# Optimization experiments

Measured on AMD Instinct MI355X. Metric: run time of the kernel, lower is better.

The kernel has to match this reference:

```python
import jax, jax.numpy as jnp
import numpy as np

B, N0, N1, FD, L, H = 4, 256, 256, 128, 3, 1
NG = N0 + N1            # nodes per graph
N = B * NG              # total nodes
EPS_BN = 1e-5
EPS_SM = 1e-16


def _build_edges():
    def perm_edges(n, off):
        idx = np.arange(n)
        a = np.repeat(idx, n); b = np.tile(idx, n)
        m = a != b
        return np.stack([a[m], b[m]]) + off
    e_intra = np.concatenate([perm_edges(N0, 0), perm_edges(N1, N0)], axis=1)
    a = np.arange(N0); b = np.arange(N0, N0 + N1)
    cross1 = np.stack([np.repeat(a, N1), np.tile(b, N0)])
    cross2 = np.stack([np.repeat(b, N0), np.tile(a, N1)])
    eg = np.concatenate([e_intra, cross1, cross2], axis=1)
    tg = np.concatenate([np.zeros(e_intra.shape[1], np.int32),
                         np.ones(cross1.shape[1] + cross2.shape[1], np.int32)])
    ei = np.concatenate([eg + g * NG for g in range(B)], axis=1).astype(np.int32)
    et = np.tile(tg, B).astype(np.int32)
    return jnp.asarray(ei), jnp.asarray(et)


def setup_inputs() -> dict:
    key = jax.random.key(0)
    ks = jax.random.split(key, 8)
    edge_index, edge_type = _build_edges()
    return {
        'desc0': jax.random.normal(ks[0], (B, FD, N0), jnp.float32),
        'desc1': jax.random.normal(ks[1], (B, FD, N1), jnp.float32),
        'W': jax.random.normal(ks[2], (L, 2, FD, H * FD), jnp.float32) * (1.0 / np.sqrt(FD)),
        'q': jax.random.normal(ks[3], (L, H * FD, H), jnp.float32) * 0.1,
        'k': jax.random.normal(ks[4], (L, H * FD, H), jnp.float32) * 0.1,
        'conv_b': jnp.zeros((L, FD), jnp.float32),
        'lin_W': jax.random.normal(ks[5], (L, FD, 2 * FD), jnp.float32) * (1.0 / np.sqrt(2 * FD)),
        'lin_b': jnp.zeros((L, FD), jnp.float32),
        'gamma': jnp.ones((L, FD), jnp.float32),
        'beta': jnp.zeros((L, FD), jnp.float32),
        'edge_index': edge_index,
        'edge_type': edge_type,
    }


def _forward(desc0, desc1, W, q, k, conv_b, lin_W, lin_b, gamma, beta, edge_index, edge_type):
    # x: [B, NG, FD] -> flattened batch graph [N, FD]
    x = jnp.concatenate([desc0, desc1], axis=2)        # [B, FD, NG]
    x = jnp.transpose(x, (0, 2, 1)).reshape(N, FD)
    src, dst = edge_index[0], edge_index[1]
    nlayers = W.shape[0]
    heads = q.shape[2]
    for l in range(nlayers):
        # relation-specific node projections (equiv to per-edge bmm with weight[edge_type])
        proj = jnp.einsum('nf,rfo->nro', x, W[l])       # [N, 2, H*FD]
        out_i = proj[dst, edge_type]                    # [E, H*FD]
        out_j = proj[src, edge_type]                    # [E, H*FD]
        alpha = jax.nn.leaky_relu(out_i @ q[l] + out_j @ k[l], 0.2)  # [E, H]
        # softmax over incoming edges of each destination node (across-relation)
        amax = jax.ops.segment_max(alpha, dst, num_segments=N)
        ex = jnp.exp(alpha - amax[dst])
        denom = jax.ops.segment_sum(ex, dst, num_segments=N)
        att = ex / (denom[dst] + EPS_SM)                # [E, H]
        msg = (att[:, :, None] * out_j.reshape(-1, heads, FD)).reshape(-1, heads * FD)
        agg = jax.ops.segment_sum(msg, dst, num_segments=N).reshape(N, heads, FD)
        m1 = jax.nn.relu(agg.mean(axis=1) + conv_b[l])  # concat=False -> mean over heads
        m2 = jnp.concatenate([x, m1], axis=1) @ lin_W[l].T + lin_b[l]
        mu = m2.mean(axis=0)
        var = ((m2 - mu) ** 2).mean(axis=0)             # biased var (BatchNorm training)
        m3 = (m2 - mu) / jnp.sqrt(var + EPS_BN) * gamma[l] + beta[l]
        x = x + m3
    x = x.reshape(B, NG, FD).transpose(0, 2, 1)         # [B, FD, NG]
    return x


def reference(desc0, desc1, W, q, k, conv_b, lin_W, lin_b, gamma, beta, edge_index, edge_type):
    x = _forward(desc0, desc1, W, q, k, conv_b, lin_W, lin_b, gamma, beta, edge_index, edge_type)
    return x[:, :, :N0], x[:, :, N0:]
```

## Files before the change

### kernel.cpp

```cpp
#include <hip/hip_runtime.h>

#define FD  128
#define NN  2048

#define OFF_X     0
#define OFF_PROJ  262144
#define OFF_QS    786432
#define OFF_KS    790528
#define OFF_SUMS  794624
#define OFF_LWT   795392
#define OFF_M2    893696

__device__ __forceinline__ int swizzle_n0(int bid) {
    int g    = (bid & 7) >> 1;
    int slot = ((bid >> 3) << 1) | (bid & 1);
    return g*512 + slot*8;
}

__device__ __forceinline__ void proj_qsks8(
    const float* __restrict__ W, const float* __restrict__ qv,
    const float* __restrict__ kv, float* __restrict__ ws,
    int l, int n0, int t, const float (*xs)[FD],
    float (*redp)[256], float* red)
{
    int kh = t >> 8, tp = t & 255;
    int rsel = tp >> 7, o = tp & 127;
    const float* Wl = W + ((size_t)(l*2 + rsel)*FD)*FD + o;
    float acc[8];
#pragma unroll
    for (int r = 0; r < 8; r++) acc[r] = 0.f;
    int kbase = kh * 64;
    for (int k4 = kbase; k4 < kbase + 64; k4 += 4) {
        float w0 = Wl[(k4+0)*FD], w1 = Wl[(k4+1)*FD];
        float w2 = Wl[(k4+2)*FD], w3 = Wl[(k4+3)*FD];
#pragma unroll
        for (int r = 0; r < 8; r++) {
            float4 xq = *(const float4*)&xs[r][k4];
            acc[r] += xq.x*w0 + xq.y*w1 + xq.z*w2 + xq.w*w3;
        }
    }
    if (kh == 1) {
#pragma unroll
        for (int r = 0; r < 8; r++) redp[r][tp] = acc[r];
    }
    __syncthreads();
    if (t < 256) {
#pragma unroll
        for (int r = 0; r < 8; r++) acc[r] += redp[r][tp];
#pragma unroll
        for (int r = 0; r < 8; r++)
            ws[OFF_PROJ + (size_t)(n0 + r)*256 + tp] = acc[r];

        float qq = qv[l*FD + o], kq = kv[l*FD + o];
        int lane = t & 63, w = t >> 6;
#pragma unroll
        for (int r = 0; r < 8; r++) {
            float vq = acc[r]*qq, vk = acc[r]*kq;
            for (int off = 32; off; off >>= 1) {
                vq += __shfl_xor(vq, off, 64);
                vk += __shfl_xor(vk, off, 64);
            }
            if (lane == 0) { red[w*16 + r*2] = vq; red[w*16 + r*2 + 1] = vk; }
        }
    }
    __syncthreads();
    if (t < 32) {
        int r = t & 7, rs = (t >> 3) & 1, wh = t >> 4;
        float v = red[(rs*2)*16 + r*2 + wh] + red[(rs*2 + 1)*16 + r*2 + wh];
        if (wh == 0) ws[OFF_QS + rs*NN + n0 + r] = v;
        else         ws[OFF_KS + rs*NN + n0 + r] = v;
    }
}

__global__ __launch_bounds__(512, 2) void k_pre(
    const float* __restrict__ d0, const float* __restrict__ d1,
    const float* __restrict__ W,  const float* __restrict__ qv,
    const float* __restrict__ kv, const float* __restrict__ linW,
    float* __restrict__ ws)
{
    int bid = blockIdx.x, t = threadIdx.x;
    if (bid >= 256) {
        if (bid < 280) {
            int vb = bid - 256;
#pragma unroll
            for (int i = 0; i < 8; i++) {
                int e = vb*4096 + i*512 + t;
                int l = e >> 15, rem = e & 32767;
                int o = rem >> 8, c = rem & 255;
                ws[OFF_LWT + l*32768 + c*FD + o] = linW[e];
            }
        } else {
            for (int i = t; i < 768; i += 512) ws[OFF_SUMS + i] = 0.f;
        }
        return;
    }
    __shared__ __attribute__((aligned(16))) float xs[8][FD];
    __shared__ float redp[8][256];
    __shared__ float red[64];
    int n0 = swizzle_n0(bid);
#pragma unroll
    for (int i = 0; i < 2; i++) {
        int idx = t + i*512;
        int row = idx >> 7, f = idx & 127;
        int n = n0 + row, gg = n >> 9, ii = n & 511;
        float v = (ii < 256) ? d0[gg*32768 + f*256 + ii]
                             : d1[gg*32768 + f*256 + (ii - 256)];
        xs[row][f] = v;
        ws[OFF_X + (size_t)n*FD + f] = v;
    }
    __syncthreads();
    proj_qsks8(W, qv, kv, ws, 0, n0, t, xs, redp, red);
}

__global__ __launch_bounds__(512, 2) void k_bp(
    const float* __restrict__ W,     const float* __restrict__ qv,
    const float* __restrict__ kv,    const float* __restrict__ gamma,
    const float* __restrict__ beta,  float* __restrict__ ws, int l)
{
    __shared__ float scale[FD], shift[FD];
    __shared__ __attribute__((aligned(16))) float xs[8][FD];
    __shared__ float redp[8][256];
    __shared__ float red[64];
    int bid = blockIdx.x, t = threadIdx.x;
    int lp = l - 1;
    if (t < 128) {
        float mu  = ws[OFF_SUMS + lp*256 + t] * (1.f/2048.f);
        float var = ws[OFF_SUMS + lp*256 + 128 + t] * (1.f/2048.f) - mu*mu;
        float rs  = rsqrtf(var + 1e-5f);
        float gm  = gamma[lp*FD + t], bt = beta[lp*FD + t];
        scale[t] = gm * rs;
        shift[t] = bt - mu * gm * rs;
    }
    __syncthreads();
    int n0 = swizzle_n0(bid);
#pragma unroll
    for (int i = 0; i < 2; i++) {
        int idx = t + i*512;
        int row = idx >> 7, f = idx & 127;
        size_t e = (size_t)(n0 + row)*FD + f;
        float xv = ws[OFF_X + e] + ws[OFF_M2 + e]*scale[f] + shift[f];
        xs[row][f] = xv;
        ws[OFF_X + e] = xv;
    }
    __syncthreads();
    proj_qsks8(W, qv, kv, ws, l, n0, t, xs, redp, red);
}

__global__ __launch_bounds__(512, 2) void k_attn(
    const float* __restrict__ convb, const float* __restrict__ linb,
    float* __restrict__ ws, int l)
{
    __shared__ __attribute__((aligned(16))) float att[8*512];
    __shared__ __attribute__((aligned(16))) float redB[8*8*128];
    __shared__ __attribute__((aligned(16))) float cat[8*256];
    __shared__ float r1[FD], r2[FD];

    int bid = blockIdx.x, t = threadIdx.x;
    int dstbase = swizzle_n0(bid);
    int g = dstbase >> 9, dloc0 = dstbase & 511;
    int Gd = (dloc0 >= 256) ? 1 : 0;

    {
        int d = t >> 6, p = t & 63;
        int dloc = dloc0 + d;
        float q0 = ws[OFF_QS + dstbase + d];
        float q1 = ws[OFF_QS + NN + dstbase + d];
        float sc[8];
#pragma unroll
        for (int j = 0; j < 8; j++) {
            int s = p + j*64;
            int ts = (s < 256) ? Gd : 1 - Gd;
            float a = (ts ? q1 : q0) + ws[OFF_KS + ts*NN + g*512 + s];
            a = a > 0.f ? a : 0.2f*a;
            sc[j] = (s == dloc) ? -1e30f : a;
        }
        float lm = sc[0];
#pragma unroll
        for (int j = 1; j < 8; j++) lm = fmaxf(lm, sc[j]);
        for (int off = 32; off; off >>= 1) lm = fmaxf(lm, __shfl_xor(lm, off, 64));
        float ex[8], lsum = 0.f;
#pragma unroll
        for (int j = 0; j < 8; j++) { ex[j] = __expf(sc[j] - lm); lsum += ex[j]; }
        for (int off = 32; off; off >>= 1) lsum += __shfl_xor(lsum, off, 64);
        float inv = 1.f / (lsum + 1e-16f);
#pragma unroll
        for (int j = 0; j < 8; j++) att[d*512 + p + j*64] = ex[j]*inv;
        if (t < 128) r1[t] = 0.f;
        else if (t < 256) r2[t - 128] = 0.f;
    }
    __syncthreads();

    int f4 = t & 31, sq = t >> 5;
    float acc[8][4];
#pragma unroll
    for (int d2 = 0; d2 < 8; d2++)
#pragma unroll
        for (int j = 0; j < 4; j++) acc[d2][j] = 0.f;
    {
        int ts = (sq < 8) ? Gd : 1 - Gd;
        const float* P = ws + OFF_PROJ + (size_t)(g*512)*256 + ts*128 + f4*4;
        int s0 = sq * 32;
#pragma unroll 4
        for (int i = 0; i < 32; i++) {
            int s = s0 + i;
            float4 p4 = *(const float4*)&P[(size_t)s*256];
#pragma unroll
            for (int d2 = 0; d2 < 8; d2++) {
                float b = att[d2*512 + s];
                acc[d2][0] += b*p4.x; acc[d2][1] += b*p4.y;
                acc[d2][2] += b*p4.z; acc[d2][3] += b*p4.w;
            }
        }
    }
    if (sq >= 8) {
#pragma unroll
        for (int d2 = 0; d2 < 8; d2++)
            *(float4*)&redB[((sq - 8)*8 + d2)*128 + f4*4] =
                make_float4(acc[d2][0], acc[d2][1], acc[d2][2], acc[d2][3]);
    }
    __syncthreads();
    if (sq < 8) {
#pragma unroll
        for (int d2 = 0; d2 < 8; d2++) {
            float4 p4 = *(const float4*)&redB[(sq*8 + d2)*128 + f4*4];
            *(float4*)&redB[(sq*8 + d2)*128 + f4*4] =
                make_float4(acc[d2][0]+p4.x, acc[d2][1]+p4.y, acc[d2][2]+p4.z, acc[d2][3]+p4.w);
        }
    }
    __syncthreads();

    {
        int dh = t >> 7, f = t & 127;
#pragma unroll
        for (int half = 0; half < 2; half++) {
            int d2 = dh + half*4;
            float agg = 0.f;
#pragma unroll
            for (int cc = 0; cc < 8; cc++) agg += redB[(cc*8 + d2)*128 + f];
            float m1v = fmaxf(agg + convb[l*FD + f], 0.f);
            cat[d2*256 + FD + f] = m1v;
            cat[d2*256 + f] = ws[OFF_X + (size_t)(dstbase + d2)*FD + f];
        }
    }
    __syncthreads();

#pragma unroll
    for (int d2 = 0; d2 < 8; d2++)
#pragma unroll
        for (int j = 0; j < 4; j++) acc[d2][j] = 0.f;
    {
        const float* lwt = ws + OFF_LWT + l*32768 + f4*4;
        int c0 = sq * 16;
#pragma unroll 4
        for (int i = 0; i < 16; i++) {
            int c = c0 + i;
            float4 w4 = *(const float4*)&lwt[c*128];
#pragma unroll
            for (int d2 = 0; d2 < 8; d2++) {
                float cv = cat[d2*256 + c];
                acc[d2][0] += cv*w4.x; acc[d2][1] += cv*w4.y;
                acc[d2][2] += cv*w4.z; acc[d2][3] += cv*w4.w;
            }
        }
    }
    if (sq >= 8) {
#pragma unroll
        for (int d2 = 0; d2 < 8; d2++)
            *(float4*)&redB[((sq - 8)*8 + d2)*128 + f4*4] =
                make_float4(acc[d2][0], acc[d2][1], acc[d2][2], acc[d2][3]);
    }
    __syncthreads();
    if (sq < 8) {
#pragma unroll
        for (int d2 = 0; d2 < 8; d2++) {
            float4 p4 = *(const float4*)&redB[(sq*8 + d2)*128 + f4*4];
            *(float4*)&redB[(sq*8 + d2)*128 + f4*4] =
                make_float4(acc[d2][0]+p4.x, acc[d2][1]+p4.y, acc[d2][2]+p4.z, acc[d2][3]+p4.w);
        }
    }
    __syncthreads();

    {
        int dh = t >> 7, o = t & 127;
        float lb = linb[l*FD + o];
#pragma unroll
        for (int half = 0; half < 2; half++) {
            int d2 = dh + half*4;
            float m2v = lb;
#pragma unroll
            for (int cc = 0; cc < 8; cc++) m2v += redB[(cc*8 + d2)*128 + o];
            ws[OFF_M2 + (size_t)(dstbase + d2)*FD + o] = m2v;
            atomicAdd(&r1[o], m2v);
            atomicAdd(&r2[o], m2v*m2v);
        }
    }
    __syncthreads();
    if (t < 128) {
        atomicAdd(&ws[OFF_SUMS + l*256 + t],       r1[t]);
        atomicAdd(&ws[OFF_SUMS + l*256 + 128 + t], r2[t]);
    }
}

__global__ __launch_bounds__(256) void k_bnout(
    const float* __restrict__ gamma, const float* __restrict__ beta,
    float* __restrict__ ws, float* __restrict__ out)
{
    __shared__ float scale[FD], shift[FD];
    int bid = blockIdx.x, t = threadIdx.x;
    if (t < 128) {
        float mu  = ws[OFF_SUMS + 2*256 + t] * (1.f/2048.f);
        float var = ws[OFF_SUMS + 2*256 + 128 + t] * (1.f/2048.f) - mu*mu;
        float rs  = rsqrtf(var + 1e-5f);
        float gm  = gamma[2*FD + t], bt = beta[2*FD + t];
        scale[t] = gm * rs;
        shift[t] = bt - mu * gm * rs;
    }
    __syncthreads();
#pragma unroll
    for (int i = 0; i < 2; i++) {
        int idx = bid*512 + i*256 + t;
        int f = idx & 127, n = idx >> 7;
        float v = ws[OFF_X + idx] + ws[OFF_M2 + idx]*scale[f] + shift[f];
        int gg = n >> 9, ii = n & 511;
        int off = (ii < 256) ? (gg*32768 + f*256 + ii)
                             : (131072 + gg*32768 + f*256 + (ii - 256));
        out[off] = v;
    }
}

extern "C" void kernel_launch(void* const* d_in, const int* in_sizes, int n_in,
                              void* d_out, int out_size, void* d_ws, size_t ws_size,
                              hipStream_t stream) {
    (void)in_sizes; (void)n_in; (void)out_size; (void)ws_size;
    const float* desc0 = (const float*)d_in[0];
    const float* desc1 = (const float*)d_in[1];
    const float* W     = (const float*)d_in[2];
    const float* q     = (const float*)d_in[3];
    const float* kk    = (const float*)d_in[4];
    const float* convb = (const float*)d_in[5];
    const float* linW  = (const float*)d_in[6];
    const float* linb  = (const float*)d_in[7];
    const float* gamma = (const float*)d_in[8];
    const float* beta  = (const float*)d_in[9];
    float* ws  = (float*)d_ws;
    float* out = (float*)d_out;

    hipLaunchKernelGGL(k_pre,  dim3(281), dim3(512), 0, stream, desc0, desc1, W, q, kk, linW, ws);
    hipLaunchKernelGGL(k_attn, dim3(256), dim3(512), 0, stream, convb, linb, ws, 0);
    hipLaunchKernelGGL(k_bp,   dim3(256), dim3(512), 0, stream, W, q, kk, gamma, beta, ws, 1);
    hipLaunchKernelGGL(k_attn, dim3(256), dim3(512), 0, stream, convb, linb, ws, 1);
    hipLaunchKernelGGL(k_bp,   dim3(256), dim3(512), 0, stream, W, q, kk, gamma, beta, ws, 2);
    hipLaunchKernelGGL(k_attn, dim3(256), dim3(512), 0, stream, convb, linb, ws, 2);
    hipLaunchKernelGGL(k_bnout, dim3(512), dim3(256), 0, stream, gamma, beta, ws, out);
}
```

Baseline: 175.7 us.

## Reassociate attention aggregation before projection and fuse layer kernels

Precomputes W·q and W·k vectors so per-node attention scores come from dot products with x, and aggregates raw x weighted by attention before applying W (att·(xW) = (att·x)W). This removes the separate projection kernel and the stored projected-node buffer, merging the BatchNorm residual update into the attention kernel with ping-pong x/m2 buffers. Each block now recomputes the BN-updated x for all 512 nodes of its graph and performs an extra 8-row matmul with W, trading redundant recomputation and more syncs for fewer launches and less global traffic.

```diff
diff --git a/kernel.cpp b/kernel.cpp
--- a/kernel.cpp
+++ b/kernel.cpp
@@ -1,15 +1,15 @@
 #include <hip/hip_runtime.h>
 
-#define FD  128
-#define NN  2048
-
-#define OFF_X     0
-#define OFF_PROJ  262144
-#define OFF_QS    786432
-#define OFF_KS    790528
-#define OFF_SUMS  794624
-#define OFF_LWT   795392
-#define OFF_M2    893696
+#define FD 128
+
+#define OFF_X0    0
+#define OFF_X1    262144
+#define OFF_M20   524288
+#define OFF_M21   786432
+#define OFF_SUMS  1048576
+#define OFF_LWT   1049344
+#define OFF_WQ    1147648
+#define OFF_WK    1148416
 
 __device__ __forceinline__ int swizzle_n0(int bid) {
     int g    = (bid & 7) >> 1;
@@ -17,160 +17,155 @@
     return g*512 + slot*8;
 }
 
-__device__ __forceinline__ void proj_qsks8(
-    const float* __restrict__ W, const float* __restrict__ qv,
-    const float* __restrict__ kv, float* __restrict__ ws,
-    int l, int n0, int t, const float (*xs)[FD],
-    float (*redp)[256], float* red)
-{
-    int kh = t >> 8, tp = t & 255;
-    int rsel = tp >> 7, o = tp & 127;
-    const float* Wl = W + ((size_t)(l*2 + rsel)*FD)*FD + o;
-    float acc[8];
-#pragma unroll
-    for (int r = 0; r < 8; r++) acc[r] = 0.f;
-    int kbase = kh * 64;
-    for (int k4 = kbase; k4 < kbase + 64; k4 += 4) {
-        float w0 = Wl[(k4+0)*FD], w1 = Wl[(k4+1)*FD];
-        float w2 = Wl[(k4+2)*FD], w3 = Wl[(k4+3)*FD];
-#pragma unroll
-        for (int r = 0; r < 8; r++) {
-            float4 xq = *(const float4*)&xs[r][k4];
-            acc[r] += xq.x*w0 + xq.y*w1 + xq.z*w2 + xq.w*w3;
-        }
-    }
-    if (kh == 1) {
-#pragma unroll
-        for (int r = 0; r < 8; r++) redp[r][tp] = acc[r];
-    }
-    __syncthreads();
-    if (t < 256) {
-#pragma unroll
-        for (int r = 0; r < 8; r++) acc[r] += redp[r][tp];
-#pragma unroll
-        for (int r = 0; r < 8; r++)
-            ws[OFF_PROJ + (size_t)(n0 + r)*256 + tp] = acc[r];
-
-        float qq = qv[l*FD + o], kq = kv[l*FD + o];
-        int lane = t & 63, w = t >> 6;
-#pragma unroll
-        for (int r = 0; r < 8; r++) {
-            float vq = acc[r]*qq, vk = acc[r]*kq;
-            for (int off = 32; off; off >>= 1) {
-                vq += __shfl_xor(vq, off, 64);
-                vk += __shfl_xor(vk, off, 64);
-            }
-            if (lane == 0) { red[w*16 + r*2] = vq; red[w*16 + r*2 + 1] = vk; }
-        }
-    }
-    __syncthreads();
-    if (t < 32) {
-        int r = t & 7, rs = (t >> 3) & 1, wh = t >> 4;
-        float v = red[(rs*2)*16 + r*2 + wh] + red[(rs*2 + 1)*16 + r*2 + wh];
-        if (wh == 0) ws[OFF_QS + rs*NN + n0 + r] = v;
-        else         ws[OFF_KS + rs*NN + n0 + r] = v;
-    }
-}
-
-__global__ __launch_bounds__(512, 2) void k_pre(
+__global__ __launch_bounds__(512) void k_pre(
     const float* __restrict__ d0, const float* __restrict__ d1,
     const float* __restrict__ W,  const float* __restrict__ qv,
     const float* __restrict__ kv, const float* __restrict__ linW,
     float* __restrict__ ws)
 {
     int bid = blockIdx.x, t = threadIdx.x;
-    if (bid >= 256) {
-        if (bid < 280) {
-            int vb = bid - 256;
-#pragma unroll
-            for (int i = 0; i < 8; i++) {
-                int e = vb*4096 + i*512 + t;
-                int l = e >> 15, rem = e & 32767;
-                int o = rem >> 8, c = rem & 255;
-                ws[OFF_LWT + l*32768 + c*FD + o] = linW[e];
-            }
-        } else {
-            for (int i = t; i < 768; i += 512) ws[OFF_SUMS + i] = 0.f;
-        }
-        return;
-    }
-    __shared__ __attribute__((aligned(16))) float xs[8][FD];
-    __shared__ float redp[8][256];
-    __shared__ float red[64];
-    int n0 = swizzle_n0(bid);
-#pragma unroll
-    for (int i = 0; i < 2; i++) {
-        int idx = t + i*512;
-        int row = idx >> 7, f = idx & 127;
-        int n = n0 + row, gg = n >> 9, ii = n & 511;
-        float v = (ii < 256) ? d0[gg*32768 + f*256 + ii]
-                             : d1[gg*32768 + f*256 + (ii - 256)];
-        xs[row][f] = v;
-        ws[OFF_X + (size_t)n*FD + f] = v;
-    }
-    __syncthreads();
-    proj_qsks8(W, qv, kv, ws, 0, n0, t, xs, redp, red);
+    if (bid < 256) {
+        int n0 = swizzle_n0(bid);
+#pragma unroll
+        for (int i = 0; i < 2; i++) {
+            int idx = t + i*512;
+            int row = idx >> 7, f = idx & 127;
+            int n = n0 + row, gg = n >> 9, ii = n & 511;
+            float v = (ii < 256) ? d0[gg*32768 + f*256 + ii]
+                                 : d1[gg*32768 + f*256 + (ii - 256)];
+            ws[OFF_X0 + (size_t)n*FD + f] = v;
+        }
+    } else if (bid < 280) {
+        int vb = bid - 256;
+#pragma unroll
+        for (int i = 0; i < 8; i++) {
+            int e = vb*4096 + i*512 + t;
+            int l = e >> 15, rem = e & 32767;
+            int o = rem >> 8, c = rem & 255;
+            ws[OFF_LWT + l*32768 + c*FD + o] = linW[e];
+        }
+    } else if (bid == 280) {
+        for (int i = t; i < 768; i += 512) ws[OFF_SUMS + i] = 0.f;
+    } else {
+        int vb = bid - 281;
+        int l = vb >> 1, r = vb & 1;
+        if (t < 128) {
+            int f = t;
+            const float* Wr = W + ((size_t)((l*2 + r)*FD + f))*FD;
+            float aq = 0.f, ak = 0.f;
+            for (int o = 0; o < 128; o++) {
+                float wv = Wr[o];
+                aq += wv * qv[l*FD + o];
+                ak += wv * kv[l*FD + o];
+            }
+            ws[OFF_WQ + (l*2 + r)*FD + f] = aq;
+            ws[OFF_WK + (l*2 + r)*FD + f] = ak;
+        }
+    }
 }
 
-__global__ __launch_bounds__(512, 2) void k_bp(
-    const float* __restrict__ W,     const float* __restrict__ qv,
-    const float* __restrict__ kv,    const float* __restrict__ gamma,
-    const float* __restrict__ beta,  float* __restrict__ ws, int l)
-{
-    __shared__ float scale[FD], shift[FD];
-    __shared__ __attribute__((aligned(16))) float xs[8][FD];
-    __shared__ float redp[8][256];
-    __shared__ float red[64];
-    int bid = blockIdx.x, t = threadIdx.x;
-    int lp = l - 1;
-    if (t < 128) {
-        float mu  = ws[OFF_SUMS + lp*256 + t] * (1.f/2048.f);
-        float var = ws[OFF_SUMS + lp*256 + 128 + t] * (1.f/2048.f) - mu*mu;
-        float rs  = rsqrtf(var + 1e-5f);
-        float gm  = gamma[lp*FD + t], bt = beta[lp*FD + t];
-        scale[t] = gm * rs;
-        shift[t] = bt - mu * gm * rs;
-    }
-    __syncthreads();
-    int n0 = swizzle_n0(bid);
-#pragma unroll
-    for (int i = 0; i < 2; i++) {
-        int idx = t + i*512;
-        int row = idx >> 7, f = idx & 127;
-        size_t e = (size_t)(n0 + row)*FD + f;
-        float xv = ws[OFF_X + e] + ws[OFF_M2 + e]*scale[f] + shift[f];
-        xs[row][f] = xv;
-        ws[OFF_X + e] = xv;
-    }
-    __syncthreads();
-    proj_qsks8(W, qv, kv, ws, l, n0, t, xs, redp, red);
-}
-
-__global__ __launch_bounds__(512, 2) void k_attn(
-    const float* __restrict__ convb, const float* __restrict__ linb,
-    float* __restrict__ ws, int l)
+__global__ __launch_bounds__(512) void k_fused(
+    const float* __restrict__ W,     const float* __restrict__ convb,
+    const float* __restrict__ linb,  const float* __restrict__ gamma,
+    const float* __restrict__ beta,  float* __restrict__ ws,
+    int l, int xin_off, int xout_off, int m2in_off, int m2out_off)
 {
     __shared__ __attribute__((aligned(16))) float att[8*512];
-    __shared__ __attribute__((aligned(16))) float redB[8*8*128];
+    __shared__ __attribute__((aligned(16))) float redB[4*8*128];
+    __shared__ __attribute__((aligned(16))) float yb[2][8][128];
     __shared__ __attribute__((aligned(16))) float cat[8*256];
-    __shared__ float r1[FD], r2[FD];
+    __shared__ __attribute__((aligned(16))) float xown[8*128];
+    __shared__ float ksv[512];
+    __shared__ float sc0[128], sh0[128];
+    __shared__ float wkA[128], wkB[128];
+    __shared__ float qsd[16];
+    __shared__ float r1[128], r2[128];
 
     int bid = blockIdx.x, t = threadIdx.x;
     int dstbase = swizzle_n0(bid);
     int g = dstbase >> 9, dloc0 = dstbase & 511;
     int Gd = (dloc0 >= 256) ? 1 : 0;
+    const float* Xin  = ws + xin_off;
+    const float* M2in = ws + m2in_off;
+    int havePrev = (l > 0);
+
+    if (t < 128) {
+        float scv = 0.f, shv = 0.f;
+        if (havePrev) {
+            float s1 = ws[OFF_SUMS + (l-1)*256 + t];
+            float s2 = ws[OFF_SUMS + (l-1)*256 + 128 + t];
+            float mu  = s1 * (1.f/2048.f);
+            float var = s2 * (1.f/2048.f) - mu*mu;
+            float rs  = rsqrtf(var + 1e-5f);
+            float gm  = gamma[(l-1)*FD + t], bt = beta[(l-1)*FD + t];
+            scv = gm*rs; shv = bt - mu*gm*rs;
+        }
+        sc0[t] = scv; sh0[t] = shv;
+        r1[t] = 0.f;  r2[t] = 0.f;
+    } else if (t < 256) {
+        int f = t - 128;
+        wkA[f] = ws[OFF_WK + (l*2 + Gd)*FD + f];
+        wkB[f] = ws[OFF_WK + (l*2 + 1 - Gd)*FD + f];
+    }
+    __syncthreads();
+
+    {
+        int w = t >> 6, lane = t & 63;
+        int li = lane & 31, sub = lane >> 5, f0 = li*4;
+        float4 cs = *(const float4*)&sc0[f0];
+        float4 sh = *(const float4*)&sh0[f0];
+        float4 ka = *(const float4*)&wkA[f0];
+        float4 kb = *(const float4*)&wkB[f0];
+        int sbeg = w*64;
+        for (int i = 0; i < 32; i++) {
+            int s = sbeg + i*2 + sub;
+            size_t base = (size_t)(g*512 + s)*FD + f0;
+            float4 x4 = *(const float4*)&Xin[base];
+            if (havePrev) {
+                float4 m4 = *(const float4*)&M2in[base];
+                x4.x += m4.x*cs.x + sh.x;
+                x4.y += m4.y*cs.y + sh.y;
+                x4.z += m4.z*cs.z + sh.z;
+                x4.w += m4.w*cs.w + sh.w;
+            }
+            float4 kk = (s < 256) ? ka : kb;
+            float d = x4.x*kk.x + x4.y*kk.y + x4.z*kk.z + x4.w*kk.w;
+            d += __shfl_xor(d, 16, 64);
+            d += __shfl_xor(d, 8, 64);
+            d += __shfl_xor(d, 4, 64);
+            d += __shfl_xor(d, 2, 64);
+            d += __shfl_xor(d, 1, 64);
+            if (li == 0) ksv[s] = d;
+            int srel = s - dloc0;
+            if (srel >= 0 && srel < 8) {
+                *(float4*)&xown[srel*FD + f0] = x4;
+                float* xo = ws + xout_off;
+                *(float4*)&xo[base] = x4;
+                float4 q0 = *(const float4*)&ws[OFF_WQ + (l*2 + 0)*FD + f0];
+                float4 q1 = *(const float4*)&ws[OFF_WQ + (l*2 + 1)*FD + f0];
+                float dq0 = x4.x*q0.x + x4.y*q0.y + x4.z*q0.z + x4.w*q0.w;
+                float dq1 = x4.x*q1.x + x4.y*q1.y + x4.z*q1.z + x4.w*q1.w;
+                dq0 += __shfl_xor(dq0, 16, 64); dq1 += __shfl_xor(dq1, 16, 64);
+                dq0 += __shfl_xor(dq0, 8, 64);  dq1 += __shfl_xor(dq1, 8, 64);
+                dq0 += __shfl_xor(dq0, 4, 64);  dq1 += __shfl_xor(dq1, 4, 64);
+                dq0 += __shfl_xor(dq0, 2, 64);  dq1 += __shfl_xor(dq1, 2, 64);
+                dq0 += __shfl_xor(dq0, 1, 64);  dq1 += __shfl_xor(dq1, 1, 64);
+                if (li == 0) { qsd[srel*2 + 0] = dq0; qsd[srel*2 + 1] = dq1; }
+            }
+        }
+    }
+    __syncthreads();
 
     {
         int d = t >> 6, p = t & 63;
         int dloc = dloc0 + d;
-        float q0 = ws[OFF_QS + dstbase + d];
-        float q1 = ws[OFF_QS + NN + dstbase + d];
+        float q0 = qsd[d*2 + 0], q1 = qsd[d*2 + 1];
         float sc[8];
 #pragma unroll
         for (int j = 0; j < 8; j++) {
             int s = p + j*64;
             int ts = (s < 256) ? Gd : 1 - Gd;
-            float a = (ts ? q1 : q0) + ws[OFF_KS + ts*NN + g*512 + s];
+            float a = (ts ? q1 : q0) + ksv[s];
             a = a > 0.f ? a : 0.2f*a;
             sc[j] = (s == dloc) ? -1e30f : a;
         }
@@ -185,119 +180,226 @@
         float inv = 1.f / (lsum + 1e-16f);
 #pragma unroll
         for (int j = 0; j < 8; j++) att[d*512 + p + j*64] = ex[j]*inv;
-        if (t < 128) r1[t] = 0.f;
-        else if (t < 256) r2[t - 128] = 0.f;
     }
     __syncthreads();
 
-    int f4 = t & 31, sq = t >> 5;
-    float acc[8][4];
-#pragma unroll
-    for (int d2 = 0; d2 < 8; d2++)
-#pragma unroll
-        for (int j = 0; j < 4; j++) acc[d2][j] = 0.f;
-    {
-        int ts = (sq < 8) ? Gd : 1 - Gd;
-        const float* P = ws + OFF_PROJ + (size_t)(g*512)*256 + ts*128 + f4*4;
-        int s0 = sq * 32;
-#pragma unroll 4
-        for (int i = 0; i < 32; i++) {
-            int s = s0 + i;
-            float4 p4 = *(const float4*)&P[(size_t)s*256];
-#pragma unroll
-            for (int d2 = 0; d2 < 8; d2++) {
-                float b = att[d2*512 + s];
-                acc[d2][0] += b*p4.x; acc[d2][1] += b*p4.y;
-                acc[d2][2] += b*p4.z; acc[d2][3] += b*p4.w;
-            }
-        }
-    }
-    if (sq >= 8) {
+    int f4 = t & 31, c = t >> 5;
+    float4 csy = *(const float4*)&sc0[f4*4];
+    float4 shy = *(const float4*)&sh0[f4*4];
+
+    for (int h = 0; h < 2; h++) {
+        float acc[8][4];
 #pragma unroll
         for (int d2 = 0; d2 < 8; d2++)
-            *(float4*)&redB[((sq - 8)*8 + d2)*128 + f4*4] =
-                make_float4(acc[d2][0], acc[d2][1], acc[d2][2], acc[d2][3]);
-    }
-    __syncthreads();
-    if (sq < 8) {
-#pragma unroll
-        for (int d2 = 0; d2 < 8; d2++) {
-            float4 p4 = *(const float4*)&redB[(sq*8 + d2)*128 + f4*4];
-            *(float4*)&redB[(sq*8 + d2)*128 + f4*4] =
-                make_float4(acc[d2][0]+p4.x, acc[d2][1]+p4.y, acc[d2][2]+p4.z, acc[d2][3]+p4.w);
-        }
-    }
-    __syncthreads();
-
-    {
-        int dh = t >> 7, f = t & 127;
-#pragma unroll
-        for (int half = 0; half < 2; half++) {
-            int d2 = dh + half*4;
-            float agg = 0.f;
-#pragma unroll
-            for (int cc = 0; cc < 8; cc++) agg += redB[(cc*8 + d2)*128 + f];
-            float m1v = fmaxf(agg + convb[l*FD + f], 0.f);
-            cat[d2*256 + FD + f] = m1v;
-            cat[d2*256 + f] = ws[OFF_X + (size_t)(dstbase + d2)*FD + f];
-        }
-    }
-    __syncthreads();
-
-#pragma unroll
-    for (int d2 = 0; d2 < 8; d2++)
-#pragma unroll
-        for (int j = 0; j < 4; j++) acc[d2][j] = 0.f;
-    {
-        const float* lwt = ws + OFF_LWT + l*32768 + f4*4;
-        int c0 = sq * 16;
+#pragma unroll
+            for (int j = 0; j < 4; j++) acc[d2][j] = 0.f;
+        const float* Xb = Xin  + (size_t)(g*512 + h*256 + c*16)*FD + f4*4;
+        const float* Mb = M2in + (size_t)(g*512 + h*256 + c*16)*FD + f4*4;
 #pragma unroll 4
         for (int i = 0; i < 16; i++) {
-            int c = c0 + i;
-            float4 w4 = *(const float4*)&lwt[c*128];
-#pragma unroll
-            for (int d2 = 0; d2 < 8; d2++) {
-                float cv = cat[d2*256 + c];
+            int s = h*256 + c*16 + i;
+            float4 x4 = *(const float4*)&Xb[(size_t)i*FD];
+            if (havePrev) {
+                float4 m4 = *(const float4*)&Mb[(size_t)i*FD];
+                x4.x += m4.x*csy.x + shy.x;
+                x4.y += m4.y*csy.y + shy.y;
+                x4.z += m4.z*csy.z + shy.z;
+                x4.w += m4.w*csy.w + shy.w;
+            }
+#pragma unroll
+            for (int d2 = 0; d2 < 8; d2++) {
+                float b = att[d2*512 + s];
+                acc[d2][0] += b*x4.x; acc[d2][1] += b*x4.y;
+                acc[d2][2] += b*x4.z; acc[d2][3] += b*x4.w;
+            }
+        }
+        if (c >= 12) {
+#pragma unroll
+            for (int d2 = 0; d2 < 8; d2++)
+                *(float4*)&redB[((c-12)*8 + d2)*128 + f4*4] =
+                    make_float4(acc[d2][0], acc[d2][1], acc[d2][2], acc[d2][3]);
+        }
+        __syncthreads();
+        if (c >= 8 && c < 12) {
+#pragma unroll
+            for (int d2 = 0; d2 < 8; d2++) {
+                float4 p4 = *(const float4*)&redB[((c-8)*8 + d2)*128 + f4*4];
+                *(float4*)&redB[((c-8)*8 + d2)*128 + f4*4] =
+                    make_float4(acc[d2][0]+p4.x, acc[d2][1]+p4.y, acc[d2][2]+p4.z, acc[d2][3]+p4.w);
+            }
+        }
+        __syncthreads();
+        if (c >= 4 && c < 8) {
+#pragma unroll
+            for (int d2 = 0; d2 < 8; d2++) {
+                float4 p4 = *(const float4*)&redB[((c-4)*8 + d2)*128 + f4*4];
+                *(float4*)&redB[((c-4)*8 + d2)*128 + f4*4] =
+                    make_float4(acc[d2][0]+p4.x, acc[d2][1]+p4.y, acc[d2][2]+p4.z, acc[d2][3]+p4.w);
+            }
+        }
+        __syncthreads();
+        if (c < 4) {
+#pragma unroll
+            for (int d2 = 0; d2 < 8; d2++) {
+                float4 p4 = *(const float4*)&redB[(c*8 + d2)*128 + f4*4];
+                *(float4*)&redB[(c*8 + d2)*128 + f4*4] =
+                    make_float4(acc[d2][0]+p4.x, acc[d2][1]+p4.y, acc[d2][2]+p4.z, acc[d2][3]+p4.w);
+            }
+        }
+        __syncthreads();
+        {
+            int dh = t >> 7, f = t & 127;
+#pragma unroll
+            for (int half2 = 0; half2 < 2; half2++) {
+                int d2 = dh + half2*4;
+                yb[h][d2][f] = redB[(0*8 + d2)*128 + f] + redB[(1*8 + d2)*128 + f]
+                             + redB[(2*8 + d2)*128 + f] + redB[(3*8 + d2)*128 + f];
+            }
+        }
+        __syncthreads();
+    }
+
+    {
+        float acc[8][4];
+#pragma unroll
+        for (int d2 = 0; d2 < 8; d2++)
+#pragma unroll
+            for (int j = 0; j < 4; j++) acc[d2][j] = 0.f;
+        int h   = (c < 8) ? 0 : 1;
+        int rel = (c < 8) ? Gd : 1 - Gd;
+        int fb  = (c & 7) * 16;
+        const float* Wm = W + ((size_t)((l*2 + rel)*FD + fb))*FD + f4*4;
+#pragma unroll 4
+        for (int i = 0; i < 16; i++) {
+            float4 w4 = *(const float4*)&Wm[(size_t)i*FD];
+#pragma unroll
+            for (int d2 = 0; d2 < 8; d2++) {
+                float yv = yb[h][d2][fb + i];
+                acc[d2][0] += yv*w4.x; acc[d2][1] += yv*w4.y;
+                acc[d2][2] += yv*w4.z; acc[d2][3] += yv*w4.w;
+            }
+        }
+        if (c >= 12) {
+#pragma unroll
+            for (int d2 = 0; d2 < 8; d2++)
+                *(float4*)&redB[((c-12)*8 + d2)*128 + f4*4] =
+                    make_float4(acc[d2][0], acc[d2][1], acc[d2][2], acc[d2][3]);
+        }
+        __syncthreads();
+        if (c >= 8 && c < 12) {
+#pragma unroll
+            for (int d2 = 0; d2 < 8; d2++) {
+                float4 p4 = *(const float4*)&redB[((c-8)*8 + d2)*128 + f4*4];
+                *(float4*)&redB[((c-8)*8 + d2)*128 + f4*4] =
+                    make_float4(acc[d2][0]+p4.x, acc[d2][1]+p4.y, acc[d2][2]+p4.z, acc[d2][3]+p4.w);
+            }
+        }
+        __syncthreads();
+        if (c >= 4 && c < 8) {
+#pragma unroll
+            for (int d2 = 0; d2 < 8; d2++) {
+                float4 p4 = *(const float4*)&redB[((c-4)*8 + d2)*128 + f4*4];
+                *(float4*)&redB[((c-4)*8 + d2)*128 + f4*4] =
+                    make_float4(acc[d2][0]+p4.x, acc[d2][1]+p4.y, acc[d2][2]+p4.z, acc[d2][3]+p4.w);
+            }
+        }
+        __syncthreads();
+        if (c < 4) {
+#pragma unroll
+            for (int d2 = 0; d2 < 8; d2++) {
+                float4 p4 = *(const float4*)&redB[(c*8 + d2)*128 + f4*4];
+                *(float4*)&redB[(c*8 + d2)*128 + f4*4] =
+                    make_float4(acc[d2][0]+p4.x, acc[d2][1]+p4.y, acc[d2][2]+p4.z, acc[d2][3]+p4.w);
+            }
+        }
+        __syncthreads();
+        {
+            int dh = t >> 7, f = t & 127;
+            float cb = convb[l*FD + f];
+#pragma unroll
+            for (int half2 = 0; half2 < 2; half2++) {
+                int d2 = dh + half2*4;
+                float aggv = redB[(0*8 + d2)*128 + f] + redB[(1*8 + d2)*128 + f]
+                           + redB[(2*8 + d2)*128 + f] + redB[(3*8 + d2)*128 + f];
+                float m1v = fmaxf(aggv + cb, 0.f);
+                cat[d2*256 + FD + f] = m1v;
+                cat[d2*256 + f]      = xown[d2*FD + f];
+            }
+        }
+        __syncthreads();
+    }
+
+    {
+        float acc[8][4];
+#pragma unroll
+        for (int d2 = 0; d2 < 8; d2++)
+#pragma unroll
+            for (int j = 0; j < 4; j++) acc[d2][j] = 0.f;
+        const float* lwt = ws + OFF_LWT + l*32768 + f4*4;
+        int c0 = c*16;
+#pragma unroll 4
+        for (int i = 0; i < 16; i++) {
+            int cc = c0 + i;
+            float4 w4 = *(const float4*)&lwt[(size_t)cc*FD];
+#pragma unroll
+            for (int d2 = 0; d2 < 8; d2++) {
+                float cv = cat[d2*256 + cc];
                 acc[d2][0] += cv*w4.x; acc[d2][1] += cv*w4.y;
                 acc[d2][2] += cv*w4.z; acc[d2][3] += cv*w4.w;
             }
         }
-    }
-    if (sq >= 8) {
-#pragma unroll
-        for (int d2 = 0; d2 < 8; d2++)
-            *(float4*)&redB[((sq - 8)*8 + d2)*128 + f4*4] =
-                make_float4(acc[d2][0], acc[d2][1], acc[d2][2], acc[d2][3]);
-    }
-    __syncthreads();
-    if (sq < 8) {
-#pragma unroll
-        for (int d2 = 0; d2 < 8; d2++) {
-            float4 p4 = *(const float4*)&redB[(sq*8 + d2)*128 + f4*4];
-            *(float4*)&redB[(sq*8 + d2)*128 + f4*4] =
-                make_float4(acc[d2][0]+p4.x, acc[d2][1]+p4.y, acc[d2][2]+p4.z, acc[d2][3]+p4.w);
-        }
-    }
-    __syncthreads();
-
-    {
-        int dh = t >> 7, o = t & 127;
-        float lb = linb[l*FD + o];
-#pragma unroll
-        for (int half = 0; half < 2; half++) {
-            int d2 = dh + half*4;
-            float m2v = lb;
-#pragma unroll
-            for (int cc = 0; cc < 8; cc++) m2v += redB[(cc*8 + d2)*128 + o];
-            ws[OFF_M2 + (size_t)(dstbase + d2)*FD + o] = m2v;
-            atomicAdd(&r1[o], m2v);
-            atomicAdd(&r2[o], m2v*m2v);
-        }
-    }
-    __syncthreads();
-    if (t < 128) {
-        atomicAdd(&ws[OFF_SUMS + l*256 + t],       r1[t]);
-        atomicAdd(&ws[OFF_SUMS + l*256 + 128 + t], r2[t]);
+        if (c >= 12) {
+#pragma unroll
+            for (int d2 = 0; d2 < 8; d2++)
+                *(float4*)&redB[((c-12)*8 + d2)*128 + f4*4] =
+                    make_float4(acc[d2][0], acc[d2][1], acc[d2][2], acc[d2][3]);
+        }
+        __syncthreads();
+        if (c >= 8 && c < 12) {
+#pragma unroll
+            for (int d2 = 0; d2 < 8; d2++) {
+                float4 p4 = *(const float4*)&redB[((c-8)*8 + d2)*128 + f4*4];
+                *(float4*)&redB[((c-8)*8 + d2)*128 + f4*4] =
+                    make_float4(acc[d2][0]+p4.x, acc[d2][1]+p4.y, acc[d2][2]+p4.z, acc[d2][3]+p4.w);
+            }
+        }
+        __syncthreads();
+        if (c >= 4 && c < 8) {
+#pragma unroll
+            for (int d2 = 0; d2 < 8; d2++) {
+                float4 p4 = *(const float4*)&redB[((c-4)*8 + d2)*128 + f4*4];
+                *(float4*)&redB[((c-4)*8 + d2)*128 + f4*4] =
+                    make_float4(acc[d2][0]+p4.x, acc[d2][1]+p4.y, acc[d2][2]+p4.z, acc[d2][3]+p4.w);
+            }
+        }
+        __syncthreads();
+        if (c < 4) {
+#pragma unroll
+            for (int d2 = 0; d2 < 8; d2++) {
+                float4 p4 = *(const float4*)&redB[(c*8 + d2)*128 + f4*4];
+                *(float4*)&redB[(c*8 + d2)*128 + f4*4] =
+                    make_float4(acc[d2][0]+p4.x, acc[d2][1]+p4.y, acc[d2][2]+p4.z, acc[d2][3]+p4.w);
+            }
+        }
+        __syncthreads();
+        {
+            int dh = t >> 7, o = t & 127;
+            float lb = linb[l*FD + o];
+#pragma unroll
+            for (int half2 = 0; half2 < 2; half2++) {
+                int d2 = dh + half2*4;
+                float m2v = lb + redB[(0*8 + d2)*128 + o] + redB[(1*8 + d2)*128 + o]
+                               + redB[(2*8 + d2)*128 + o] + redB[(3*8 + d2)*128 + o];
+                ws[m2out_off + (size_t)(dstbase + d2)*FD + o] = m2v;
+                atomicAdd(&r1[o], m2v);
+                atomicAdd(&r2[o], m2v*m2v);
+            }
+        }
+        __syncthreads();
+        if (t < 128) {
+            atomicAdd(&ws[OFF_SUMS + l*256 + t],       r1[t]);
+            atomicAdd(&ws[OFF_SUMS + l*256 + 128 + t], r2[t]);
+        }
     }
 }
 
@@ -320,7 +422,7 @@
     for (int i = 0; i < 2; i++) {
         int idx = bid*512 + i*256 + t;
         int f = idx & 127, n = idx >> 7;
-        float v = ws[OFF_X + idx] + ws[OFF_M2 + idx]*scale[f] + shift[f];
+        float v = ws[OFF_X0 + idx] + ws[OFF_M20 + idx]*scale[f] + shift[f];
         int gg = n >> 9, ii = n & 511;
         int off = (ii < 256) ? (gg*32768 + f*256 + ii)
                              : (131072 + gg*32768 + f*256 + (ii - 256));
@@ -345,11 +447,17 @@
     float* ws  = (float*)d_ws;
     float* out = (float*)d_out;
 
-    hipLaunchKernelGGL(k_pre,  dim3(281), dim3(512), 0, stream, desc0, desc1, W, q, kk, linW, ws);
-    hipLaunchKernelGGL(k_attn, dim3(256), dim3(512), 0, stream, convb, linb, ws, 0);
-    hipLaunchKernelGGL(k_bp,   dim3(256), dim3(512), 0, stream, W, q, kk, gamma, beta, ws, 1);
-    hipLaunchKernelGGL(k_attn, dim3(256), dim3(512), 0, stream, convb, linb, ws, 1);
-    hipLaunchKernelGGL(k_bp,   dim3(256), dim3(512), 0, stream, W, q, kk, gamma, beta, ws, 2);
-    hipLaunchKernelGGL(k_attn, dim3(256), dim3(512), 0, stream, convb, linb, ws, 2);
-    hipLaunchKernelGGL(k_bnout, dim3(512), dim3(256), 0, stream, gamma, beta, ws, out);
+    hipLaunchKernelGGL(k_pre, dim3(287), dim3(512), 0, stream,
+                       desc0, desc1, W, q, kk, linW, ws);
+    hipLaunchKernelGGL(k_fused, dim3(256), dim3(512), 0, stream,
+                       W, convb, linb, gamma, beta, ws,
+                       0, OFF_X0, OFF_X1, OFF_M20, OFF_M20);
+    hipLaunchKernelGGL(k_fused, dim3(256), dim3(512), 0, stream,
+                       W, convb, linb, gamma, beta, ws,
+                       1, OFF_X0, OFF_X1, OFF_M20, OFF_M21);
+    hipLaunchKernelGGL(k_fused, dim3(256), dim3(512), 0, stream,
+                       W, convb, linb, gamma, beta, ws,
+                       2, OFF_X1, OFF_X0, OFF_M21, OFF_M20);
+    hipLaunchKernelGGL(k_bnout, dim3(512), dim3(256), 0, stream,
+                       gamma, beta, ws, out);
 }
```

Result: slower. 214.4 us (+22.0%).
